# Kernel tuning notes

Measured on AMD Instinct MI355X. Metric: run time of the kernel, lower is better.

Reference implementation:

```python
import jax, jax.numpy as jnp
import numpy as np
import math

N = 12288
IN_MAIN, IN_MOD = 64, 128
NC_INNER, NC_QK, OUT_MAIN = 16, 8, 64

def setup_inputs() -> dict:
    key = jax.random.key(0)
    ks = jax.random.split(key, 8)
    s = lambda fan_in: 1.0 / np.sqrt(fan_in)
    return {
        "x_main": jax.random.normal(ks[0], (N, IN_MAIN), dtype=jnp.float32),
        "x_mod": jax.random.normal(ks[1], (N, IN_MOD), dtype=jnp.float32),
        "xyz": jax.random.uniform(ks[2], (N, 3), dtype=jnp.float32),
        # MLP E: [in_main+in_mod -> nc_inner -> nc_inner], bias=False (weights stored [in, out])
        "W_e1": jax.random.uniform(ks[3], (IN_MAIN + IN_MOD, NC_INNER), jnp.float32, -s(IN_MAIN + IN_MOD), s(IN_MAIN + IN_MOD)),
        "W_e2": jax.random.uniform(ks[4], (NC_INNER, NC_INNER), jnp.float32, -s(NC_INNER), s(NC_INNER)),
        "W_q": jax.random.uniform(ks[5], (NC_INNER, NC_QK), jnp.float32, -s(NC_INNER), s(NC_INNER)),
        "W_k": jax.random.uniform(ks[6], (NC_INNER, NC_QK), jnp.float32, -s(NC_INNER), s(NC_INNER)),
        "W_v": jax.random.uniform(ks[7], (NC_INNER, OUT_MAIN), jnp.float32, -s(NC_INNER), s(NC_INNER)),
    }

def reference(x_main, x_mod, xyz, W_e1, W_e2, W_q, W_k, W_v):
    # concat 3D + 2D features: [N, in_main+in_mod]
    x = jnp.concatenate((x_main, x_mod), axis=-1)
    # MLP E (bias-free Linear + ReLU per layer): [N, nc_inner]
    h = jax.nn.relu(jax.nn.relu(x @ W_e1) @ W_e2)
    Q = h @ W_q  # [N, nc_qk]
    K = h @ W_k  # [N, nc_qk]
    V = h @ W_v  # [N, out_main]
    scale = 1.0 / math.sqrt(NC_QK)
    scores = (Q @ K.T) * scale          # [N, N] full global attention
    attn = jax.nn.softmax(scores, axis=1)
    return attn @ V                     # [N, out_main]
```

## Files before the change

kernel.cpp:

```cpp
#include <hip/hip_runtime.h>
#include <stdint.h>


#define NN 12288

typedef float    f32x16 __attribute__((ext_vector_type(16)));
typedef short    s16x8  __attribute__((ext_vector_type(8)));
typedef unsigned short u16;

#define MFMA_32x32x16_BF16 __builtin_amdgcn_mfma_f32_32x32x16_bf16

#define OFF_QB   0u
#define OFF_KB   196608u
#define OFF_VT   393216u
#define OFF_PO   2162688u

typedef __attribute__((address_space(3))) void lds_void_t;
typedef const __attribute__((address_space(1))) void gbl_void_t;
__device__ __forceinline__ void gld16(const void* g, void* l) {
    __builtin_amdgcn_global_load_lds((gbl_void_t*)g, (lds_void_t*)l, 16, 0, 0);
}

__device__ __forceinline__ float bf2f(u16 s) {
    union { unsigned int u; float f; } c; c.u = ((unsigned int)s) << 16; return c.f;
}
__device__ __forceinline__ u16 f2bf(float f) {
    union { float f; unsigned int u; } c; c.f = f;
    return (u16)((c.u + 0x8000u) >> 16);
}
__device__ __forceinline__ unsigned int pk2(float a, float b) {
    union { float f; unsigned int u; } ca, cb; ca.f = a; cb.f = b;
    return ((ca.u + 0x8000u) >> 16) | ((cb.u + 0x8000u) & 0xffff0000u);
}
__device__ __forceinline__ unsigned int pkbf(float a, float b) {
#if __has_builtin(__builtin_amdgcn_cvt_pk_bf16_f32)
    auto r = __builtin_amdgcn_cvt_pk_bf16_f32(a, b);
    union { decltype(r) v; unsigned int u; } c; c.v = r; return c.u;
#else
    return pk2(a, b);
#endif
}
__device__ __forceinline__ f32x16 zf16() {
    f32x16 z;
#pragma unroll
    for (int i = 0; i < 16; ++i) z[i] = 0.f;
    return z;
}
__device__ __forceinline__ s16x8 zs8() {
    s16x8 z;
#pragma unroll
    for (int i = 0; i < 8; ++i) z[i] = 0;
    return z;
}

union U8 { s16x8 v; unsigned int u[4]; };

__global__ __launch_bounds__(256) void k1_qkv(
    const void* __restrict__ xmain, const void* __restrict__ xmod,
    const void* __restrict__ we1, const void* __restrict__ we2,
    const void* __restrict__ wqp, const void* __restrict__ wkp,
    const void* __restrict__ wvp,
    u16* __restrict__ qb, u16* __restrict__ kb, u16* __restrict__ vt)
{
    __shared__ float wf[4608];
    __shared__ int   sflag;
    __shared__ float lh1[64][4][17];
    __shared__ float lh2[64][17];

    const int t = threadIdx.x;
    const int r = t >> 2;
    const int p = t & 3;
    const int row = blockIdx.x * 64 + r;

    if (t == 0) sflag = 0;
    __syncthreads();
    {
        float v = bf2f(((const u16*)xmod)[2 * t]);
        if (fabsf(v) > 16.f) atomicAdd(&sflag, 1);
    }
    __syncthreads();
    const int isf32 = (sflag > 8);

    const float SCL = 0.51006979f;
    if (isf32) {
        const float* a1 = (const float*)we1; const float* a2 = (const float*)we2;
        const float* aq = (const float*)wqp; const float* ak = (const float*)wkp;
        const float* av = (const float*)wvp;
        for (int i = t; i < 4608; i += 256) {
            if      (i < 3072) wf[i] = a1[i];
            else if (i < 3328) wf[i] = a2[i - 3072];
            else if (i < 3456) wf[i] = aq[i - 3328] * SCL;
            else if (i < 3584) wf[i] = ak[i - 3456];
            else               wf[i] = av[i - 3584];
        }
    } else {
        const u16* a1 = (const u16*)we1; const u16* a2 = (const u16*)we2;
        const u16* aq = (const u16*)wqp; const u16* ak = (const u16*)wkp;
        const u16* av = (const u16*)wvp;
        for (int i = t; i < 4608; i += 256) {
            if      (i < 3072) wf[i] = bf2f(a1[i]);
            else if (i < 3328) wf[i] = bf2f(a2[i - 3072]);
            else if (i < 3456) wf[i] = bf2f(aq[i - 3328]) * SCL;
            else if (i < 3584) wf[i] = bf2f(ak[i - 3456]);
            else               wf[i] = bf2f(av[i - 3584]);
        }
    }
    __syncthreads();

    const float* __restrict__ W1 = wf;
    const float* __restrict__ W2 = wf + 3072;
    const float* __restrict__ Wq = wf + 3328;
    const float* __restrict__ Wk = wf + 3456;
    const float* __restrict__ Wv = wf + 3584;

    float h1p[16];
#pragma unroll
    for (int o = 0; o < 16; ++o) h1p[o] = 0.f;

    if (isf32) {
#pragma unroll
        for (int cc = 0; cc < 12; ++cc) {
            const int c = p + cc * 4;
            float4 xv = (c < 16)
                ? ((const float4*)xmain)[(size_t)row * 16 + c]
                : ((const float4*)xmod)[(size_t)row * 32 + (c - 16)];
            float xs[4] = {xv.x, xv.y, xv.z, xv.w};
#pragma unroll
            for (int j = 0; j < 4; ++j) {
                const float* wr = W1 + (c * 4 + j) * 16;
#pragma unroll
                for (int o = 0; o < 16; ++o) h1p[o] += xs[j] * wr[o];
            }
        }
    } else {
#pragma unroll
        for (int cc = 0; cc < 12; ++cc) {
            const int c = p + cc * 4;
            uint2 xv = (c < 16)
                ? ((const uint2*)xmain)[(size_t)row * 16 + c]
                : ((const uint2*)xmod)[(size_t)row * 32 + (c - 16)];
            float xs[4] = { bf2f((u16)(xv.x & 0xffff)), bf2f((u16)(xv.x >> 16)),
                            bf2f((u16)(xv.y & 0xffff)), bf2f((u16)(xv.y >> 16)) };
#pragma unroll
            for (int j = 0; j < 4; ++j) {
                const float* wr = W1 + (c * 4 + j) * 16;
#pragma unroll
                for (int o = 0; o < 16; ++o) h1p[o] += xs[j] * wr[o];
            }
        }
    }
#pragma unroll
    for (int o = 0; o < 16; ++o) lh1[r][p][o] = h1p[o];
    __syncthreads();

    float h1[16];
#pragma unroll
    for (int o = 0; o < 16; ++o)
        h1[o] = fmaxf(lh1[r][0][o] + lh1[r][1][o] + lh1[r][2][o] + lh1[r][3][o], 0.f);

#pragma unroll
    for (int oo = 0; oo < 4; ++oo) {
        const int o = p * 4 + oo;
        float s = 0.f;
#pragma unroll
        for (int j = 0; j < 16; ++j) s += h1[j] * W2[j * 16 + o];
        lh2[r][o] = fmaxf(s, 0.f);
    }
    __syncthreads();

    float h2[16];
#pragma unroll
    for (int j = 0; j < 16; ++j) h2[j] = lh2[r][j];

    {
        float q0 = 0.f, q1 = 0.f, k0 = 0.f, k1 = 0.f;
        const int o = 2 * p;
#pragma unroll
        for (int j = 0; j < 16; ++j) {
            q0 += h2[j] * Wq[j * 8 + o];
            q1 += h2[j] * Wq[j * 8 + o + 1];
            k0 += h2[j] * Wk[j * 8 + o];
            k1 += h2[j] * Wk[j * 8 + o + 1];
        }
        ((unsigned int*)qb)[(size_t)row * 4 + p] = pk2(q0, q1);
        ((unsigned int*)kb)[(size_t)row * 4 + p] = pk2(k0, k1);
    }

    const int tI = row >> 5, kk = row & 31;
#pragma unroll
    for (int c16 = 0; c16 < 16; ++c16) {
        const int c = p * 16 + c16;
        float v = 0.f;
#pragma unroll
        for (int j = 0; j < 16; ++j) v += h2[j] * Wv[j * 64 + c];
        vt[(size_t)tI * 2304 + c * 36 + kk] = f2bf(v);
    }
}


__device__ __forceinline__ void tile_pv(
    const f32x16& S, const u16* __restrict__ base, int l31, int half,
    const s16x8& ones, f32x16& acc0, f32x16& acc1, f32x16& accl)
{
    float pr[16];
#pragma unroll
    for (int r = 0; r < 16; ++r) pr[r] = __builtin_amdgcn_exp2f(S[r]);

    U8 p0, p1;
#pragma unroll
    for (int i = 0; i < 4; ++i) {
        p0.u[i] = pkbf(pr[2 * i],     pr[2 * i + 1]);
        p1.u[i] = pkbf(pr[8 + 2 * i], pr[8 + 2 * i + 1]);
    }

    accl = MFMA_32x32x16_BF16(ones, p0.v, accl, 0, 0, 0);
    accl = MFMA_32x32x16_BF16(ones, p1.v, accl, 0, 0, 0);

    const u16* r0 = base + l31 * 36 + 4 * half;
    const u16* r1 = base + (32 + l31) * 36 + 4 * half;
    U8 va;
    uint2 x0, x1;
    x0 = *(const uint2*)(r0);       x1 = *(const uint2*)(r0 + 8);
    va.u[0] = x0.x; va.u[1] = x0.y; va.u[2] = x1.x; va.u[3] = x1.y;
    acc0 = MFMA_32x32x16_BF16(va.v, p0.v, acc0, 0, 0, 0);
    x0 = *(const uint2*)(r1);       x1 = *(const uint2*)(r1 + 8);
    va.u[0] = x0.x; va.u[1] = x0.y; va.u[2] = x1.x; va.u[3] = x1.y;
    acc1 = MFMA_32x32x16_BF16(va.v, p0.v, acc1, 0, 0, 0);
    x0 = *(const uint2*)(r0 + 16);  x1 = *(const uint2*)(r0 + 24);
    va.u[0] = x0.x; va.u[1] = x0.y; va.u[2] = x1.x; va.u[3] = x1.y;
    acc0 = MFMA_32x32x16_BF16(va.v, p1.v, acc0, 0, 0, 0);
    x0 = *(const uint2*)(r1 + 16);  x1 = *(const uint2*)(r1 + 24);
    va.u[0] = x0.x; va.u[1] = x0.y; va.u[2] = x1.x; va.u[3] = x1.y;
    acc1 = MFMA_32x32x16_BF16(va.v, p1.v, acc1, 0, 0, 0);
}

__global__ __launch_bounds__(256, 4) void k2_attn(
    const u16* __restrict__ qb, const u16* __restrict__ kb,
    const u16* __restrict__ vt,
    u16* __restrict__ po, float* __restrict__ pl,
    int nsplit, int niter)
{
    __shared__ union SM {
        uint4 stage[2][576];
        float sf[2304];
    } sm;

    const int tid  = threadIdx.x;
    const int lane = tid & 63;
    const int half = lane >> 5;
    const int l31  = lane & 31;
    const int w    = tid >> 6;
    const int qB   = (blockIdx.x % 96) * 128;
    const int sp   = blockIdx.x / 96;
    const int myq  = qB + 32 * w;
    const int key_start = sp * (NN / nsplit);
    const int c0 = key_start >> 6;

    const f32x16 Z = zf16();
    s16x8 qf = zs8();
    if (!half) qf = *(const s16x8*)(qb + (size_t)(myq + l31) * 8);

    s16x8 ones;
#pragma unroll
    for (int i = 0; i < 8; ++i) ones[i] = (short)0x3F80;

    f32x16 acc0 = Z, acc1 = Z, accl = Z;

    {
        const char* g = (const char*)vt + (size_t)c0 * 9216 + 2304 * w + lane * 16;
        char* l = (char*)&sm.stage[0][0] + 2304 * w;
        gld16(g, l);
        gld16(g + 1024, l + 1024);
        if (lane < 16) gld16(g + 2048, l + 2048);
    }
    const s16x8* kp = (const s16x8*)kb;
    s16x8 ka_c0 = kp[key_start + l31];
    s16x8 ka_c1 = kp[key_start + 32 + l31];

    for (int it = 0; it < niter; ++it) {
        __builtin_amdgcn_s_waitcnt(0x0F70);
        __syncthreads();
        const int cb = it & 1;
        const bool has_next = (it + 1 < niter);

        s16x8 ka_n0, ka_n1;
        if (has_next) {
            const int nk = key_start + (it + 1) * 64 + l31;
            ka_n0 = kp[nk];
            ka_n1 = kp[nk + 32];
            const char* g = (const char*)vt + (size_t)(c0 + it + 1) * 9216
                          + 2304 * w + lane * 16;
            char* l = (char*)&sm.stage[cb ^ 1][0] + 2304 * w;
            gld16(g, l);
            gld16(g + 1024, l + 1024);
            if (lane < 16) gld16(g + 2048, l + 2048);
        }

        const u16* baseA = (const u16*)&sm.stage[cb][0];

        {
            f32x16 Sa = MFMA_32x32x16_BF16(ka_c0, qf, Z, 0, 0, 0);
            tile_pv(Sa, baseA, l31, half, ones, acc0, acc1, accl);
        }
        {
            f32x16 Sb = MFMA_32x32x16_BF16(ka_c1, qf, Z, 0, 0, 0);
            tile_pv(Sb, baseA + 2304, l31, half, ones, acc0, acc1, accl);
        }

        if (has_next) { ka_c0 = ka_n0; ka_c1 = ka_n1; }
    }

    const float ls = accl[0];

    u16* poS = po + (size_t)sp * (NN * 64);
    for (int j = 0; j < 4; ++j) {
        __syncthreads();
        if (w == j) {
#pragma unroll
            for (int r = 0; r < 16; ++r) {
                const int c = (r & 3) + 8 * (r >> 2) + 4 * half;
                sm.sf[c * 33 + l31]        = acc0[r];
                sm.sf[(32 + c) * 33 + l31] = acc1[r];
            }
            if (lane < 32) sm.sf[2112 + l31] = ls;
        }
        __syncthreads();
        const int rq = tid >> 3;
        const int c0b = (tid & 7) * 8;
        unsigned int u0 = pkbf(sm.sf[(c0b + 0) * 33 + rq], sm.sf[(c0b + 1) * 33 + rq]);
        unsigned int u1 = pkbf(sm.sf[(c0b + 2) * 33 + rq], sm.sf[(c0b + 3) * 33 + rq]);
        unsigned int u2 = pkbf(sm.sf[(c0b + 4) * 33 + rq], sm.sf[(c0b + 5) * 33 + rq]);
        unsigned int u3 = pkbf(sm.sf[(c0b + 6) * 33 + rq], sm.sf[(c0b + 7) * 33 + rq]);
        *(uint4*)(poS + (size_t)(qB + 32 * j + rq) * 64 + c0b) =
            make_uint4(u0, u1, u2, u3);
        if (tid < 32)
            pl[(size_t)sp * NN + qB + 32 * j + tid] = sm.sf[2112 + tid];
    }
}

__global__ __launch_bounds__(256) void k3_norm(
    const u16* __restrict__ po, const float* __restrict__ pl,
    float4* __restrict__ out, int nsplit)
{
    const int i = blockIdx.x * 256 + threadIdx.x;
    const int row = i >> 4;
    const int c0 = (i & 15) * 4;
    float l = 0.f;
    float o0 = 0.f, o1 = 0.f, o2 = 0.f, o3 = 0.f;
    for (int s = 0; s < nsplit; ++s) {
        l += pl[(size_t)s * NN + row];
        uint2 p = *(const uint2*)(po + (size_t)s * (NN * 64) +
                                  (size_t)row * 64 + c0);
        o0 += bf2f((u16)(p.x & 0xffff)); o1 += bf2f((u16)(p.x >> 16));
        o2 += bf2f((u16)(p.y & 0xffff)); o3 += bf2f((u16)(p.y >> 16));
    }
    const float rl = 1.0f / l;
    out[i] = make_float4(o0 * rl, o1 * rl, o2 * rl, o3 * rl);
}

extern "C" void kernel_launch(void* const* d_in, const int* in_sizes, int n_in,
                              void* d_out, int out_size, void* d_ws, size_t ws_size,
                              hipStream_t stream)
{
    const void* xmain = d_in[0];
    const void* xmod  = d_in[1];
    const void* we1   = d_in[3];
    const void* we2   = d_in[4];
    const void* wq    = d_in[5];
    const void* wk    = d_in[6];
    const void* wv    = d_in[7];

    char* ws = (char*)d_ws;
    u16*   qb   = (u16*)  (ws + OFF_QB);
    u16*   kb   = (u16*)  (ws + OFF_KB);
    u16*   vt   = (u16*)  (ws + OFF_VT);

    int S = 1;
    for (int cand = 16; cand >= 1; cand >>= 1) {
        size_t need = (size_t)OFF_PO + (size_t)cand * (NN * 64 * 2) +
                      (size_t)cand * (NN * 4);
        if (ws_size >= need) { S = cand; break; }
    }
    u16*   po = (u16*)(ws + OFF_PO);
    float* pl = (float*)(ws + OFF_PO + (size_t)S * (NN * 64 * 2));
    const int niter = NN / (64 * S);

    k1_qkv<<<192, 256, 0, stream>>>(xmain, xmod, we1, we2, wq, wk, wv,
                                    qb, kb, vt);
    k2_attn<<<96 * S, 256, 0, stream>>>(qb, kb, vt, po, pl, S, niter);
    k3_norm<<<768, 256, 0, stream>>>(po, pl, (float4*)d_out, S);
}
```

Baseline: 130.9 us.

## Interleave K into V chunk layout and deepen LDS pipeline to four stages

K is now written into the same per-64-key chunk as transposed V, so each chunk is one contiguous 10240-byte block loaded into LDS by async global-to-LDS copies. This removes the separate per-lane global loads of K. The attention loop moves from a double buffer to a four-buffer ring with three chunks in flight, using explicit vmcnt waits and raw barriers to hide load latency. The cost is more LDS per block, which could lower occupancy, and a more fragile wait-count scheme.

Result: no change. 130.0 us (-0.7%).

```diff
diff --git a/kernel.cpp b/kernel.cpp
--- a/kernel.cpp
+++ b/kernel.cpp
@@ -11,9 +11,10 @@
 #define MFMA_32x32x16_BF16 __builtin_amdgcn_mfma_f32_32x32x16_bf16
 
 #define OFF_QB   0u
-#define OFF_KB   196608u
-#define OFF_VT   393216u
+#define OFF_VT   196608u
 #define OFF_PO   2162688u
+
+#define VMCNT(n) (0x0F70 | (n))
 
 typedef __attribute__((address_space(3))) void lds_void_t;
 typedef const __attribute__((address_space(1))) void gbl_void_t;
@@ -60,7 +61,7 @@
     const void* __restrict__ we1, const void* __restrict__ we2,
     const void* __restrict__ wqp, const void* __restrict__ wkp,
     const void* __restrict__ wvp,
-    u16* __restrict__ qb, u16* __restrict__ kb, u16* __restrict__ vt)
+    u16* __restrict__ qb, u16* __restrict__ vt)
 {
     __shared__ float wf[4608];
     __shared__ int   sflag;
@@ -183,17 +184,18 @@
             k1 += h2[j] * Wk[j * 8 + o + 1];
         }
         ((unsigned int*)qb)[(size_t)row * 4 + p] = pk2(q0, q1);
-        ((unsigned int*)kb)[(size_t)row * 4 + p] = pk2(k0, k1);
-    }
-
-    const int tI = row >> 5, kk = row & 31;
+        ((unsigned int*)vt)[(size_t)(row >> 6) * 2560 + 2304 +
+                            (row & 63) * 4 + p] = pk2(k0, k1);
+    }
+
+    const int ch = row >> 6, tI = (row >> 5) & 1, kk = row & 31;
 #pragma unroll
     for (int c16 = 0; c16 < 16; ++c16) {
         const int c = p * 16 + c16;
         float v = 0.f;
 #pragma unroll
         for (int j = 0; j < 16; ++j) v += h2[j] * Wv[j * 64 + c];
-        vt[(size_t)tI * 2304 + c * 36 + kk] = f2bf(v);
+        vt[(size_t)ch * 5120 + tI * 2304 + c * 36 + kk] = f2bf(v);
     }
 }
 
@@ -234,14 +236,30 @@
     acc1 = MFMA_32x32x16_BF16(va.v, p1.v, acc1, 0, 0, 0);
 }
 
+__device__ __forceinline__ void chunk_body(
+    const u16* __restrict__ base, const s16x8& qf, const s16x8& ones,
+    int l31, int half, f32x16& acc0, f32x16& acc1, f32x16& accl)
+{
+    const f32x16 Z = zf16();
+    s16x8 ka0 = *(const s16x8*)(base + 4608 + l31 * 8);
+    s16x8 ka1 = *(const s16x8*)(base + 4864 + l31 * 8);
+    {
+        f32x16 Sa = MFMA_32x32x16_BF16(ka0, qf, Z, 0, 0, 0);
+        tile_pv(Sa, base, l31, half, ones, acc0, acc1, accl);
+    }
+    {
+        f32x16 Sb = MFMA_32x32x16_BF16(ka1, qf, Z, 0, 0, 0);
+        tile_pv(Sb, base + 2304, l31, half, ones, acc0, acc1, accl);
+    }
+}
+
 __global__ __launch_bounds__(256, 4) void k2_attn(
-    const u16* __restrict__ qb, const u16* __restrict__ kb,
-    const u16* __restrict__ vt,
+    const u16* __restrict__ qb, const u16* __restrict__ vt,
     u16* __restrict__ po, float* __restrict__ pl,
     int nsplit, int niter)
 {
     __shared__ union SM {
-        uint4 stage[2][576];
+        uint4 stage[4][640];
         float sf[2304];
     } sm;
 
@@ -254,7 +272,7 @@
     const int sp   = blockIdx.x / 96;
     const int myq  = qB + 32 * w;
     const int key_start = sp * (NN / nsplit);
-    const int c0 = key_start >> 6;
+    const int ch0 = key_start >> 6;
 
     const f32x16 Z = zf16();
     s16x8 qf = zs8();
@@ -266,49 +284,42 @@
 
     f32x16 acc0 = Z, acc1 = Z, accl = Z;
 
-    {
-        const char* g = (const char*)vt + (size_t)c0 * 9216 + 2304 * w + lane * 16;
-        char* l = (char*)&sm.stage[0][0] + 2304 * w;
+    auto STAGE = [&](int c, int b) {
+        const char* g = (const char*)vt + (size_t)(ch0 + c) * 10240
+                      + 2560 * w + lane * 16;
+        char* l = (char*)&sm.stage[b][0] + 2560 * w;
         gld16(g, l);
         gld16(g + 1024, l + 1024);
-        if (lane < 16) gld16(g + 2048, l + 2048);
-    }
-    const s16x8* kp = (const s16x8*)kb;
-    s16x8 ka_c0 = kp[key_start + l31];
-    s16x8 ka_c1 = kp[key_start + 32 + l31];
-
-    for (int it = 0; it < niter; ++it) {
-        __builtin_amdgcn_s_waitcnt(0x0F70);
-        __syncthreads();
-        const int cb = it & 1;
-        const bool has_next = (it + 1 < niter);
-
-        s16x8 ka_n0, ka_n1;
-        if (has_next) {
-            const int nk = key_start + (it + 1) * 64 + l31;
-            ka_n0 = kp[nk];
-            ka_n1 = kp[nk + 32];
-            const char* g = (const char*)vt + (size_t)(c0 + it + 1) * 9216
-                          + 2304 * w + lane * 16;
-            char* l = (char*)&sm.stage[cb ^ 1][0] + 2304 * w;
-            gld16(g, l);
-            gld16(g + 1024, l + 1024);
-            if (lane < 16) gld16(g + 2048, l + 2048);
-        }
-
-        const u16* baseA = (const u16*)&sm.stage[cb][0];
-
-        {
-            f32x16 Sa = MFMA_32x32x16_BF16(ka_c0, qf, Z, 0, 0, 0);
-            tile_pv(Sa, baseA, l31, half, ones, acc0, acc1, accl);
-        }
-        {
-            f32x16 Sb = MFMA_32x32x16_BF16(ka_c1, qf, Z, 0, 0, 0);
-            tile_pv(Sb, baseA + 2304, l31, half, ones, acc0, acc1, accl);
-        }
-
-        if (has_next) { ka_c0 = ka_n0; ka_c1 = ka_n1; }
-    }
+        if (lane < 32) gld16(g + 2048, l + 2048);
+    };
+
+    STAGE(0, 0);
+    STAGE(1, 1);
+    STAGE(2, 2);
+
+    int it = 0;
+    for (; it + 2 < niter; ++it) {
+        __builtin_amdgcn_sched_barrier(0);
+        __builtin_amdgcn_s_waitcnt(VMCNT(6));
+        __builtin_amdgcn_s_barrier();
+        __builtin_amdgcn_sched_barrier(0);
+        if (it + 3 < niter) STAGE(it + 3, (it + 3) & 3);
+        chunk_body((const u16*)&sm.stage[it & 3][0], qf, ones,
+                   l31, half, acc0, acc1, accl);
+    }
+    __builtin_amdgcn_sched_barrier(0);
+    __builtin_amdgcn_s_waitcnt(VMCNT(3));
+    __builtin_amdgcn_s_barrier();
+    __builtin_amdgcn_sched_barrier(0);
+    chunk_body((const u16*)&sm.stage[it & 3][0], qf, ones,
+               l31, half, acc0, acc1, accl);
+    ++it;
+    __builtin_amdgcn_sched_barrier(0);
+    __builtin_amdgcn_s_waitcnt(VMCNT(0));
+    __builtin_amdgcn_s_barrier();
+    __builtin_amdgcn_sched_barrier(0);
+    chunk_body((const u16*)&sm.stage[it & 3][0], qf, ones,
+               l31, half, acc0, acc1, accl);
 
     const float ls = accl[0];
 
@@ -372,7 +383,6 @@
 
     char* ws = (char*)d_ws;
     u16*   qb   = (u16*)  (ws + OFF_QB);
-    u16*   kb   = (u16*)  (ws + OFF_KB);
     u16*   vt   = (u16*)  (ws + OFF_VT);
 
     int S = 1;
@@ -386,7 +396,7 @@
     const int niter = NN / (64 * S);
 
     k1_qkv<<<192, 256, 0, stream>>>(xmain, xmod, we1, we2, wq, wk, wv,
-                                    qb, kb, vt);
-    k2_attn<<<96 * S, 256, 0, stream>>>(qb, kb, vt, po, pl, S, niter);
+                                    qb, vt);
+    k2_attn<<<96 * S, 256, 0, stream>>>(qb, vt, po, pl, S, niter);
     k3_norm<<<768, 256, 0, stream>>>(po, pl, (float4*)d_out, S);
 }
```
